# Kernel optimization log

Hardware: AMD Instinct MI355X
Metric: run time of the kernel (lower is better)

The kernel has to match this reference:

```python
import jax, jax.numpy as jnp
import numpy as np

EPS = 1e-15
BALL_EPS = 1e-5  # geoopt-style clamp away from the ball boundary


def expmap0(u):
    # Poincare ball (curvature -1): expmap0(u) = tanh(||u||) * u / ||u||
    n = jnp.linalg.norm(u, axis=-1, keepdims=True)
    n = jnp.maximum(n, EPS)
    return jnp.tanh(n) * u / n


def setup_inputs() -> dict:
    key = jax.random.key(0)
    k1, k2, k3 = jax.random.split(key, 3)
    B, H, D, L = 32768, 768, 384, 128
    cls_output = jax.random.normal(k1, (B, H), dtype=jnp.float32)
    W_proj = jax.random.normal(k2, (H, D), dtype=jnp.float32) * 0.02
    b_proj = jnp.zeros((D,), dtype=jnp.float32)
    # class prototypes: uniform(-0.1, 0.1) then expmap0, as in __init__
    tangent = jax.random.uniform(k3, (L, D), dtype=jnp.float32, minval=-0.1, maxval=0.1)
    poincare_weight = expmap0(tangent)
    return {"cls_output": cls_output, "W_proj": W_proj, "b_proj": b_proj,
            "poincare_weight": poincare_weight}


def reference(cls_output, W_proj, b_proj, poincare_weight):
    # projection (dropout is identity in eval mode)
    projected = cls_output @ W_proj + b_proj            # [B, D]
    x = expmap0(projected)                              # [B, D] points in ball
    y = poincare_weight                                 # [L, D] class reps in ball
    # Poincare distance for all (B, L) pairs, fused via dot products:
    # ||(-x) mobius+ y||^2 = ||x - y||^2 / (1 - 2<x,y> + ||x||^2 ||y||^2)
    x2 = jnp.sum(x * x, axis=-1)                        # [B]
    y2 = jnp.sum(y * y, axis=-1)                        # [L]
    xy = x @ y.T                                        # [B, L]
    sq_diff = x2[:, None] + y2[None, :] - 2.0 * xy      # ||x - y||^2
    denom = 1.0 - 2.0 * xy + x2[:, None] * y2[None, :]
    ratio = jnp.clip(sq_diff / denom, 0.0, (1.0 - BALL_EPS) ** 2)
    dist = 2.0 * jnp.arctanh(jnp.sqrt(ratio))           # [B, L]
    logits = -dist
    return logits, x
```

## Files before the change

kernel.cpp:

```cpp
#include <hip/hip_runtime.h>

typedef __attribute__((ext_vector_type(8))) short bf16x8;
typedef __attribute__((ext_vector_type(16))) float f32x16;

__device__ __forceinline__ unsigned short f2b(float f) {
  unsigned x = __builtin_bit_cast(unsigned, f);
  x += 0x7fffu + ((x >> 16) & 1u);
  return (unsigned short)(x >> 16);
}

__global__ __launch_bounds__(256) void k_prep(const float* __restrict__ W,
                                              const float* __restrict__ Y,
                                              unsigned short* __restrict__ Wt,
                                              unsigned short* __restrict__ Ybf,
                                              float* __restrict__ y2) {
  __shared__ unsigned short sT[64][72];
  int b = blockIdx.x;
  if (b < 72) {
    int bk = (b % 12) * 64, bn = (b / 12) * 64;
    int c = threadIdx.x & 63, rr = threadIdx.x >> 6;
#pragma unroll
    for (int i = 0; i < 16; i++) {
      int row = rr * 16 + i;
      sT[row][c] = f2b(W[(size_t)(bk + row) * 384 + bn + c]);
    }
    __syncthreads();
#pragma unroll
    for (int i = 0; i < 16; i++) {
      int row = rr * 16 + i;
      Wt[(size_t)(bn + row) * 768 + bk + c] = sT[c][row];
    }
  } else {
    int t = threadIdx.x;
    for (int i = t; i < 12288; i += 256) {
      float4 v = ((const float4*)Y)[i];
      ushort4 o;
      o.x = f2b(v.x); o.y = f2b(v.y); o.z = f2b(v.z); o.w = f2b(v.w);
      ((ushort4*)Ybf)[i] = o;
    }
    if (t < 128) {
      const float4* row = (const float4*)(Y + (size_t)t * 384);
      float s = 0.f;
#pragma unroll
      for (int j = 0; j < 96; j++) {
        float4 v = row[j];
        s += v.x * v.x + v.y * v.y + v.z * v.z + v.w * v.w;
      }
      y2[t] = s;
    }
  }
}

#define LDS1 72
#define LDSX 392

__global__ __launch_bounds__(512, 4) void k_main(const float* __restrict__ cls,
                                                 const unsigned short* __restrict__ Wt,
                                                 const float* __restrict__ bias,
                                                 const unsigned short* __restrict__ Ybf,
                                                 const float* __restrict__ y2,
                                                 float* __restrict__ xout,
                                                 float* __restrict__ out) {
  __shared__ __align__(16) unsigned short sm[32256];
  __shared__ float rs[64][4];
  __shared__ float sF[64];
  __shared__ float sQ[64];

  unsigned short* sA = sm;
  unsigned short* sW = sm + 4608;
  unsigned short* sX = sm;

  const int tid = threadIdx.x;
  const int bm = blockIdx.x * 64;
  const int wave = tid >> 6, lane = tid & 63;
  const int r = lane & 31, h = lane >> 5;
  const int rg = wave & 1, cg = wave >> 1;

  f32x16 acc[3];
#pragma unroll
  for (int j = 0; j < 3; j++)
#pragma unroll
    for (int e = 0; e < 16; e++) acc[j][e] = 0.f;

  const int arow = tid >> 3, akc = tid & 7;

  float4 rA0, rA1;
  {
    const float* src = cls + (size_t)(bm + arow) * 768 + akc * 8;
    rA0 = *(const float4*)(src);
    rA1 = *(const float4*)(src + 4);
  }

  for (int t = 0; t < 12; t++) {
    const int k0 = t * 64;
    asm volatile("s_waitcnt lgkmcnt(0)" ::: "memory");
    __builtin_amdgcn_s_barrier();

    uint4 rW[6];
#pragma unroll
    for (int it = 0; it < 6; it++) {
      int c = tid + it * 512, row = c >> 3, kc = c & 7;
      rW[it] = *(const uint4*)(Wt + (size_t)row * 768 + k0 + kc * 8);
    }

    {
      uint4 p;
      p.x = (unsigned)f2b(rA0.x) | ((unsigned)f2b(rA0.y) << 16);
      p.y = (unsigned)f2b(rA0.z) | ((unsigned)f2b(rA0.w) << 16);
      p.z = (unsigned)f2b(rA1.x) | ((unsigned)f2b(rA1.y) << 16);
      p.w = (unsigned)f2b(rA1.z) | ((unsigned)f2b(rA1.w) << 16);
      *(uint4*)(sA + arow * LDS1 + akc * 8) = p;
    }
#pragma unroll
    for (int it = 0; it < 6; it++) {
      int c = tid + it * 512, row = c >> 3, kc = c & 7;
      *(uint4*)(sW + row * LDS1 + kc * 8) = rW[it];
    }

    if (t < 11) {
      const float* src = cls + (size_t)(bm + arow) * 768 + k0 + 64 + akc * 8;
      rA0 = *(const float4*)(src);
      rA1 = *(const float4*)(src + 4);
    }

    asm volatile("s_waitcnt lgkmcnt(0)" ::: "memory");
    __builtin_amdgcn_s_barrier();

#pragma unroll
    for (int sub = 0; sub < 4; sub++) {
      const int kk = sub * 16 + h * 8;
      bf16x8 a  = *(const bf16x8*)(sA + (rg * 32 + r) * LDS1 + kk);
      bf16x8 b0 = *(const bf16x8*)(sW + (cg * 96 + r) * LDS1 + kk);
      bf16x8 b1 = *(const bf16x8*)(sW + (cg * 96 + 32 + r) * LDS1 + kk);
      bf16x8 b2 = *(const bf16x8*)(sW + (cg * 96 + 64 + r) * LDS1 + kk);
      acc[0] = __builtin_amdgcn_mfma_f32_32x32x16_bf16(a, b0, acc[0], 0, 0, 0);
      acc[1] = __builtin_amdgcn_mfma_f32_32x32x16_bf16(a, b1, acc[1], 0, 0, 0);
      acc[2] = __builtin_amdgcn_mfma_f32_32x32x16_bf16(a, b2, acc[2], 0, 0, 0);
    }
  }

  float bcol[3];
#pragma unroll
  for (int j = 0; j < 3; j++) bcol[j] = bias[cg * 96 + j * 32 + r];

#pragma unroll
  for (int reg = 0; reg < 16; reg++) {
    float s = 0.f;
#pragma unroll
    for (int j = 0; j < 3; j++) {
      float v = acc[j][reg] + bcol[j];
      acc[j][reg] = v;
      s += v * v;
    }
    s += __shfl_xor(s, 1);
    s += __shfl_xor(s, 2);
    s += __shfl_xor(s, 4);
    s += __shfl_xor(s, 8);
    s += __shfl_xor(s, 16);
    if (r == 0) {
      int rowl = rg * 32 + (reg & 3) + 8 * (reg >> 2) + 4 * h;
      rs[rowl][cg] = s;
    }
  }
  asm volatile("s_waitcnt lgkmcnt(0)" ::: "memory");
  __builtin_amdgcn_s_barrier();
  if (tid < 64) {
    float n2 = rs[tid][0] + rs[tid][1] + rs[tid][2] + rs[tid][3];
    float n = fmaxf(sqrtf(n2), 1e-15f);
    float f = tanhf(n) / n;
    sF[tid] = f;
    sQ[tid] = n2 * f * f;
  }
  asm volatile("s_waitcnt lgkmcnt(0)" ::: "memory");
  __builtin_amdgcn_s_barrier();

#pragma unroll
  for (int reg = 0; reg < 16; reg++) {
    int rowl = rg * 32 + (reg & 3) + 8 * (reg >> 2) + 4 * h;
    float f = sF[rowl];
#pragma unroll
    for (int j = 0; j < 3; j++) {
      float v = acc[j][reg] * f;
      int col = cg * 96 + j * 32 + r;
      xout[(size_t)(bm + rowl) * 384 + col] = v;
      sX[rowl * LDSX + col] = f2b(v);
    }
  }

  asm volatile("s_waitcnt lgkmcnt(0)" ::: "memory");
  __builtin_amdgcn_s_barrier();

  const int rt = (wave & 1) * 32, ct = (wave >> 1) * 32;
  f32x16 acc2;
#pragma unroll
  for (int e = 0; e < 16; e++) acc2[e] = 0.f;

  for (int cc = 0; cc < 6; cc++) {
#pragma unroll
    for (int sub = 0; sub < 4; sub++) {
      const int kk = cc * 64 + sub * 16 + h * 8;
      bf16x8 a = *(const bf16x8*)(sX + (rt + r) * LDSX + kk);
      bf16x8 b = *(const bf16x8*)(Ybf + (size_t)(ct + r) * 384 + kk);
      acc2 = __builtin_amdgcn_mfma_f32_32x32x16_bf16(a, b, acc2, 0, 0, 0);
    }
  }

  const float CLIP = 0.9999800001f;
  float yc = y2[ct + r];
#pragma unroll
  for (int reg = 0; reg < 16; reg++) {
    int rowl = rt + (reg & 3) + 8 * (reg >> 2) + 4 * h;
    float xr = sQ[rowl];
    float xy = acc2[reg];
    float sq = xr + yc - 2.f * xy;
    float den = 1.f - 2.f * xy + xr * yc;
    float ratio = fminf(fmaxf(sq / den, 0.f), CLIP);
    float s = sqrtf(ratio);
    float dist = logf((1.f + s) / (1.f - s));
    out[(size_t)(bm + rowl) * 128 + ct + r] = -dist;
  }
}

extern "C" void kernel_launch(void* const* d_in, const int* in_sizes, int n_in,
                              void* d_out, int out_size, void* d_ws, size_t ws_size,
                              hipStream_t stream) {
  const float* cls  = (const float*)d_in[0];
  const float* W    = (const float*)d_in[1];
  const float* bias = (const float*)d_in[2];
  const float* Y    = (const float*)d_in[3];

  float* out_logits = (float*)d_out;
  float* out_x = out_logits + (size_t)32768 * 128;

  float* x2 = (float*)d_ws;
  float* y2 = x2 + 32768;
  unsigned short* Wt = (unsigned short*)(y2 + 128);
  unsigned short* Ybf = Wt + (size_t)384 * 768;

  k_prep<<<73, 256, 0, stream>>>(W, Y, Wt, Ybf, y2);
  k_main<<<512, 512, 0, stream>>>(cls, Wt, bias, Ybf, y2, out_x, out_logits);
}
```

Baseline: 218.9 us.

## Double-buffer W via global_load_lds DMA with 128-row tiles and fragment layout

Reorganises the prep kernel so W is stored in a per-k-tile fragment-major bf16 layout that can be copied straight into LDS. The main kernel doubles the row tile to 128 with 1024 threads, loads W tiles asynchronously with global_load_lds into double-buffered LDS, and prefetches the A rows two steps ahead. This removes one barrier per k-step and the register round trip for W, so loads overlap with MFMA work. In exchange it uses about 135KB of LDS per block, which lowers occupancy, and halves the grid to 256 blocks.

```diff
diff --git a/kernel.cpp b/kernel.cpp
--- a/kernel.cpp
+++ b/kernel.cpp
@@ -7,6 +7,12 @@
   unsigned x = __builtin_bit_cast(unsigned, f);
   x += 0x7fffu + ((x >> 16) & 1u);
   return (unsigned short)(x >> 16);
+}
+
+__device__ __forceinline__ void dma16(const unsigned short* g, unsigned short* l) {
+  __builtin_amdgcn_global_load_lds(
+      (const __attribute__((address_space(1))) unsigned int*)g,
+      (__attribute__((address_space(3))) unsigned int*)l, 16, 0, 0);
 }
 
 __global__ __launch_bounds__(256) void k_prep(const float* __restrict__ W,
@@ -14,22 +20,23 @@
                                               unsigned short* __restrict__ Wt,
                                               unsigned short* __restrict__ Ybf,
                                               float* __restrict__ y2) {
-  __shared__ unsigned short sT[64][72];
   int b = blockIdx.x;
-  if (b < 72) {
-    int bk = (b % 12) * 64, bn = (b / 12) * 64;
-    int c = threadIdx.x & 63, rr = threadIdx.x >> 6;
-#pragma unroll
-    for (int i = 0; i < 16; i++) {
-      int row = rr * 16 + i;
-      sT[row][c] = f2b(W[(size_t)(bk + row) * 384 + bn + c]);
-    }
-    __syncthreads();
-#pragma unroll
-    for (int i = 0; i < 16; i++) {
-      int row = rr * 16 + i;
-      Wt[(size_t)(bn + row) * 768 + bk + c] = sT[c][row];
-    }
+  if (b < 144) {
+    int fid = b * 256 + threadIdx.x;
+    int kt  = fid / 3072;
+    int rem = fid - kt * 3072;
+    int sh  = rem / 384;
+    int n   = rem - sh * 384;
+    const float* src = W + (size_t)(kt * 64 + sh * 8) * 384 + n;
+    unsigned short o[8];
+#pragma unroll
+    for (int i = 0; i < 8; i++) o[i] = f2b(src[(size_t)i * 384]);
+    uint4 p;
+    p.x = (unsigned)o[0] | ((unsigned)o[1] << 16);
+    p.y = (unsigned)o[2] | ((unsigned)o[3] << 16);
+    p.z = (unsigned)o[4] | ((unsigned)o[5] << 16);
+    p.w = (unsigned)o[6] | ((unsigned)o[7] << 16);
+    *(uint4*)(Wt + (size_t)fid * 8) = p;
   } else {
     int t = threadIdx.x;
     for (int i = t; i < 12288; i += 256) {
@@ -51,30 +58,26 @@
   }
 }
 
-#define LDS1 72
+#define LDSA 72
 #define LDSX 392
 
-__global__ __launch_bounds__(512, 4) void k_main(const float* __restrict__ cls,
-                                                 const unsigned short* __restrict__ Wt,
-                                                 const float* __restrict__ bias,
-                                                 const unsigned short* __restrict__ Ybf,
-                                                 const float* __restrict__ y2,
-                                                 float* __restrict__ xout,
-                                                 float* __restrict__ out) {
-  __shared__ __align__(16) unsigned short sm[32256];
-  __shared__ float rs[64][4];
-  __shared__ float sF[64];
-  __shared__ float sQ[64];
-
-  unsigned short* sA = sm;
-  unsigned short* sW = sm + 4608;
-  unsigned short* sX = sm;
+__global__ __launch_bounds__(1024, 4) void k_main(const float* __restrict__ cls,
+                                                  const unsigned short* __restrict__ Wt,
+                                                  const float* __restrict__ bias,
+                                                  const unsigned short* __restrict__ Ybf,
+                                                  const float* __restrict__ y2,
+                                                  float* __restrict__ xout,
+                                                  float* __restrict__ out) {
+  __shared__ __align__(16) unsigned short sm[67584];
+  __shared__ float rs[128][4];
+  __shared__ float sF[128];
+  __shared__ float sQ[128];
 
   const int tid = threadIdx.x;
-  const int bm = blockIdx.x * 64;
+  const int bm = blockIdx.x * 128;
   const int wave = tid >> 6, lane = tid & 63;
   const int r = lane & 31, h = lane >> 5;
-  const int rg = wave & 1, cg = wave >> 1;
+  const int rg = wave & 3, cg = wave >> 2;
 
   f32x16 acc[3];
 #pragma unroll
@@ -83,56 +86,58 @@
     for (int e = 0; e < 16; e++) acc[j][e] = 0.f;
 
   const int arow = tid >> 3, akc = tid & 7;
-
-  float4 rA0, rA1;
+  const float* asrc = cls + (size_t)(bm + arow) * 768 + akc * 8;
+
   {
-    const float* src = cls + (size_t)(bm + arow) * 768 + akc * 8;
-    rA0 = *(const float4*)(src);
-    rA1 = *(const float4*)(src + 4);
-  }
-
+    unsigned short* wdst = sm + 18432;
+    const unsigned short* wsrc = Wt;
+#pragma unroll
+    for (int i = 0; i < 3; i++) {
+      int fb = (wave * 3 + i) * 64;
+      dma16(wsrc + (size_t)(fb + lane) * 8, wdst + fb * 8);
+    }
+  }
+  float4 rA[2][2];
+  rA[0][0] = *(const float4*)(asrc);
+  rA[0][1] = *(const float4*)(asrc + 4);
+  rA[1][0] = *(const float4*)(asrc + 64);
+  rA[1][1] = *(const float4*)(asrc + 68);
+
+#pragma unroll
   for (int t = 0; t < 12; t++) {
-    const int k0 = t * 64;
-    asm volatile("s_waitcnt lgkmcnt(0)" ::: "memory");
-    __builtin_amdgcn_s_barrier();
-
-    uint4 rW[6];
-#pragma unroll
-    for (int it = 0; it < 6; it++) {
-      int c = tid + it * 512, row = c >> 3, kc = c & 7;
-      rW[it] = *(const uint4*)(Wt + (size_t)row * 768 + k0 + kc * 8);
-    }
-
     {
       uint4 p;
-      p.x = (unsigned)f2b(rA0.x) | ((unsigned)f2b(rA0.y) << 16);
-      p.y = (unsigned)f2b(rA0.z) | ((unsigned)f2b(rA0.w) << 16);
-      p.z = (unsigned)f2b(rA1.x) | ((unsigned)f2b(rA1.y) << 16);
-      p.w = (unsigned)f2b(rA1.z) | ((unsigned)f2b(rA1.w) << 16);
-      *(uint4*)(sA + arow * LDS1 + akc * 8) = p;
-    }
-#pragma unroll
-    for (int it = 0; it < 6; it++) {
-      int c = tid + it * 512, row = c >> 3, kc = c & 7;
-      *(uint4*)(sW + row * LDS1 + kc * 8) = rW[it];
-    }
-
-    if (t < 11) {
-      const float* src = cls + (size_t)(bm + arow) * 768 + k0 + 64 + akc * 8;
-      rA0 = *(const float4*)(src);
-      rA1 = *(const float4*)(src + 4);
-    }
-
-    asm volatile("s_waitcnt lgkmcnt(0)" ::: "memory");
+      p.x = (unsigned)f2b(rA[t & 1][0].x) | ((unsigned)f2b(rA[t & 1][0].y) << 16);
+      p.y = (unsigned)f2b(rA[t & 1][0].z) | ((unsigned)f2b(rA[t & 1][0].w) << 16);
+      p.z = (unsigned)f2b(rA[t & 1][1].x) | ((unsigned)f2b(rA[t & 1][1].y) << 16);
+      p.w = (unsigned)f2b(rA[t & 1][1].z) | ((unsigned)f2b(rA[t & 1][1].w) << 16);
+      *(uint4*)(sm + (t & 1) * 9216 + arow * LDSA + akc * 8) = p;
+    }
+    if (t < 11) asm volatile("s_waitcnt vmcnt(2) lgkmcnt(0)" ::: "memory");
+    else        asm volatile("s_waitcnt vmcnt(0) lgkmcnt(0)" ::: "memory");
     __builtin_amdgcn_s_barrier();
-
-#pragma unroll
-    for (int sub = 0; sub < 4; sub++) {
-      const int kk = sub * 16 + h * 8;
-      bf16x8 a  = *(const bf16x8*)(sA + (rg * 32 + r) * LDS1 + kk);
-      bf16x8 b0 = *(const bf16x8*)(sW + (cg * 96 + r) * LDS1 + kk);
-      bf16x8 b1 = *(const bf16x8*)(sW + (cg * 96 + 32 + r) * LDS1 + kk);
-      bf16x8 b2 = *(const bf16x8*)(sW + (cg * 96 + 64 + r) * LDS1 + kk);
+    if (t + 1 < 12) {
+      unsigned short* wdst = sm + 18432 + ((t + 1) & 1) * 24576;
+      const unsigned short* wsrc = Wt + (size_t)(t + 1) * 3072 * 8;
+#pragma unroll
+      for (int i = 0; i < 3; i++) {
+        int fb = (wave * 3 + i) * 64;
+        dma16(wsrc + (size_t)(fb + lane) * 8, wdst + fb * 8);
+      }
+    }
+    if (t + 2 < 12) {
+      rA[t & 1][0] = *(const float4*)(asrc + (t + 2) * 64);
+      rA[t & 1][1] = *(const float4*)(asrc + (t + 2) * 64 + 4);
+    }
+    const unsigned short* ab = sm + (t & 1) * 9216;
+    const unsigned short* wb = sm + 18432 + (t & 1) * 24576;
+#pragma unroll
+    for (int s = 0; s < 4; s++) {
+      bf16x8 a = *(const bf16x8*)(ab + (rg * 32 + r) * LDSA + s * 16 + h * 8);
+      const unsigned short* wf = wb + (size_t)((s * 2 + h) * 384) * 8;
+      bf16x8 b0 = *(const bf16x8*)(wf + (size_t)(cg * 96 + r) * 8);
+      bf16x8 b1 = *(const bf16x8*)(wf + (size_t)(cg * 96 + 32 + r) * 8);
+      bf16x8 b2 = *(const bf16x8*)(wf + (size_t)(cg * 96 + 64 + r) * 8);
       acc[0] = __builtin_amdgcn_mfma_f32_32x32x16_bf16(a, b0, acc[0], 0, 0, 0);
       acc[1] = __builtin_amdgcn_mfma_f32_32x32x16_bf16(a, b1, acc[1], 0, 0, 0);
       acc[2] = __builtin_amdgcn_mfma_f32_32x32x16_bf16(a, b2, acc[2], 0, 0, 0);
@@ -164,7 +169,7 @@
   }
   asm volatile("s_waitcnt lgkmcnt(0)" ::: "memory");
   __builtin_amdgcn_s_barrier();
-  if (tid < 64) {
+  if (tid < 128) {
     float n2 = rs[tid][0] + rs[tid][1] + rs[tid][2] + rs[tid][3];
     float n = fmaxf(sqrtf(n2), 1e-15f);
     float f = tanhf(n) / n;
@@ -183,23 +188,23 @@
       float v = acc[j][reg] * f;
       int col = cg * 96 + j * 32 + r;
       xout[(size_t)(bm + rowl) * 384 + col] = v;
-      sX[rowl * LDSX + col] = f2b(v);
-    }
-  }
-
+      sm[rowl * LDSX + col] = f2b(v);
+    }
+  }
   asm volatile("s_waitcnt lgkmcnt(0)" ::: "memory");
   __builtin_amdgcn_s_barrier();
 
-  const int rt = (wave & 1) * 32, ct = (wave >> 1) * 32;
+  const int rt = (wave & 3) * 32, ct = (wave >> 2) * 32;
   f32x16 acc2;
 #pragma unroll
   for (int e = 0; e < 16; e++) acc2[e] = 0.f;
 
+#pragma unroll
   for (int cc = 0; cc < 6; cc++) {
 #pragma unroll
     for (int sub = 0; sub < 4; sub++) {
       const int kk = cc * 64 + sub * 16 + h * 8;
-      bf16x8 a = *(const bf16x8*)(sX + (rt + r) * LDSX + kk);
+      bf16x8 a = *(const bf16x8*)(sm + (rt + r) * LDSX + kk);
       bf16x8 b = *(const bf16x8*)(Ybf + (size_t)(ct + r) * 384 + kk);
       acc2 = __builtin_amdgcn_mfma_f32_32x32x16_bf16(a, b, acc2, 0, 0, 0);
     }
@@ -237,6 +242,6 @@
   unsigned short* Wt = (unsigned short*)(y2 + 128);
   unsigned short* Ybf = Wt + (size_t)384 * 768;
 
-  k_prep<<<73, 256, 0, stream>>>(W, Y, Wt, Ybf, y2);
-  k_main<<<512, 512, 0, stream>>>(cls, Wt, bias, Ybf, y2, out_x, out_logits);
-}
+  k_prep<<<145, 256, 0, stream>>>(W, Y, Wt, Ybf, y2);
+  k_main<<<256, 1024, 0, stream>>>(cls, Wt, bias, Ybf, y2, out_x, out_logits);
+}
```

New measurement: 213.4 us. 1.03x faster.
